# Performance work log

Measured on AMD Instinct MI355X. Metric: run time of the kernel, lower is better.

## Reference

```python
import jax, jax.numpy as jnp
import numpy as np

STRIDE = 16
NUM_A = 9
POS_TH, NEG_TH = 0.7, 0.3
FG, BG, IGN = 1.0, 0.0, 2.0
CAP = 128  # BATCH_SIZE * 0.5 for both fg and bg


def _generate_base_anchors(base_size=16, ratios=(0.5, 1.0, 2.0), scales=(8, 16, 32)):
    w = h = float(base_size)
    xc = yc = 0.5 * (base_size - 1)
    size = w * h
    out = []
    for r in ratios:
        ws = np.round(np.sqrt(size / r))
        hs = np.round(ws * r)
        for s in scales:
            W, H = ws * s, hs * s
            out.append([xc - 0.5 * (W - 1), yc - 0.5 * (H - 1),
                        xc + 0.5 * (W - 1), yc + 0.5 * (H - 1)])
    return np.asarray(out, dtype=np.float32)  # [9,4]


def _all_anchors(H, W):
    base = _generate_base_anchors()
    sx = np.arange(W, dtype=np.float32) * STRIDE
    sy = np.arange(H, dtype=np.float32) * STRIDE
    xs, ys = np.meshgrid(sx, sy)  # row-major over (h, w)
    shifts = np.stack([xs.ravel(), ys.ravel(), xs.ravel(), ys.ravel()], 1)
    return jnp.asarray((shifts[:, None, :] + base[None, :, :]).reshape(-1, 4))  # [H*W*9,4], order (h,w,a)


def _forward(scores, gt, im_w, im_h):
    H, W = scores.shape[2], scores.shape[3]
    anchors = _all_anchors(H, W)  # [N,4]
    valid = (anchors[:, 0] >= 0.) & (anchors[:, 1] >= 0.) & \
            (anchors[:, 2] < im_w) & (anchors[:, 3] < im_h)
    # pairwise IoU with +1 box convention
    aw = anchors[:, 2] - anchors[:, 0] + 1.
    ah = anchors[:, 3] - anchors[:, 1] + 1.
    a_area = jnp.where((aw > 0) & (ah > 0), aw * ah, 0.)
    gw = gt[:, 2] - gt[:, 0] + 1.
    gh = gt[:, 3] - gt[:, 1] + 1.
    g_area = jnp.where((gw > 0) & (gh > 0), gw * gh, 0.)
    ix1 = jnp.maximum(anchors[:, None, 0], gt[None, :, 0])
    iy1 = jnp.maximum(anchors[:, None, 1], gt[None, :, 1])
    ix2 = jnp.minimum(anchors[:, None, 2], gt[None, :, 2])
    iy2 = jnp.minimum(anchors[:, None, 3], gt[None, :, 3])
    iw = ix2 - ix1 + 1.
    ih = iy2 - iy1 + 1.
    inter = jnp.where((iw > 0) & (ih > 0), iw * ih, 0.)
    ovl = inter / (a_area[:, None] + g_area[None, :] - inter)  # [N,G]
    ovl_m = jnp.where(valid[:, None], ovl, -1.)  # exclude invalid anchors
    a_argmax = jnp.argmax(ovl, axis=1)           # best gt per anchor
    a_max = jnp.max(ovl, axis=1)
    g_max = jnp.max(ovl_m, axis=0)               # best (valid) anchor overlap per gt
    gt_fg = jnp.any(ovl_m == g_max[None, :], axis=1) & valid
    labels = jnp.where(valid & (a_max < NEG_TH), BG, IGN)
    labels = jnp.where(gt_fg, FG, labels)
    labels = jnp.where(valid & (a_max >= POS_TH), FG, labels)
    # random subsample fg/bg down to CAP each (matches npr.choice semantics in distribution)
    kf, kb = jax.random.split(jax.random.key(42))
    def subsample(lbl, mask, k):
        s = jnp.where(mask, jax.random.uniform(k, lbl.shape), jnp.inf)
        ranks = jnp.argsort(jnp.argsort(s))
        keep = ranks < jnp.minimum(jnp.sum(mask), CAP)
        return jnp.where(mask & ~keep, IGN, lbl)
    labels = subsample(labels, labels == FG, kf)
    labels = subsample(labels, labels == BG, kb)
    num_ni = jnp.sum(labels != IGN).astype(jnp.float32)
    gts = gt[a_argmax]
    ax = (anchors[:, 2] + anchors[:, 0]) * 0.5
    ay = (anchors[:, 3] + anchors[:, 1]) * 0.5
    gwm = gts[:, 2] - gts[:, 0] + 1.
    ghm = gts[:, 3] - gts[:, 1] + 1.
    gx = (gts[:, 2] + gts[:, 0]) * 0.5
    gy = (gts[:, 3] + gts[:, 1]) * 0.5
    adj = jnp.stack([(gx - ax) / aw, (gy - ay) / ah,
                     jnp.log(gwm / aw), jnp.log(ghm / ah)], axis=1)  # [N,4]
    adj = jnp.where(valid[:, None], adj, 0.)
    wts = jnp.where((labels == FG)[:, None], 1.0 / num_ni, 0.) * jnp.ones((1, 4), jnp.float32)
    labels_out = labels.reshape(1, H, W, NUM_A).transpose(0, 3, 1, 2) \
                       .reshape(1, 1, NUM_A * H, W).astype(jnp.int32)
    adj_out = adj.reshape(1, H, W, 4 * NUM_A).transpose(0, 3, 1, 2)
    wts_out = wts.reshape(1, H, W, 4 * NUM_A).transpose(0, 3, 1, 2)
    return labels_out, adj_out, wts_out


def setup_inputs() -> dict:
    key = jax.random.key(0)
    k1, k2, k3 = jax.random.split(key, 3)
    scores = jax.random.normal(k1, (1, 18, 256, 256), dtype=jnp.float32)
    G = 64
    cxy = jax.random.uniform(k2, (G, 2), minval=100., maxval=3900.)
    wh = jax.random.uniform(k3, (G, 2), minval=32., maxval=512.)
    x1y1 = jnp.clip(cxy - wh * 0.5, 0., 4095.)
    x2y2 = jnp.clip(cxy + wh * 0.5, 0., 4095.)
    gt = jnp.concatenate([x1y1, x2y2], axis=1)  # [G,4] = x1,y1,x2,y2
    return {"anchor_object_scores": scores, "ground_truth_boxes": gt,
            "im_w": 4096, "im_h": 4096}


def reference(anchor_object_scores, ground_truth_boxes, im_w, im_h):
    return _forward(anchor_object_scores, ground_truth_boxes, im_w, im_h)
```

## Files before the change

kernel.cpp:

```cpp
#include <hip/hip_runtime.h>
#include <stdint.h>


#define NUM_A 9
#define HW 65536
#define N_ANCH 589824
#define NG 64
#define CAPK 128u
#define NBIN 2048
#define BIN_SHIFT 12
#define CAND_CAP 2048

#define LAB_BG 0u
#define LAB_FG 1u
#define LAB_IGN 2u

#define OFF_HF    0
#define OFF_HB    NBIN
#define OFF_CNTF  (2*NBIN)
#define OFF_CNTB  (OFF_CNTF + 1)
#define OFF_ROOT1 (OFF_CNTF + 2)
#define OFF_ROOT2 (OFF_CNTF + 3)
#define OFF_SEL   (OFF_CNTF + 4)
#define OFF_SUB1  4112
#define OFF_SUB2  (OFF_SUB1 + 32*16)
#define CTRL_WORDS (OFF_SUB2 + 64*16)
#define OFF_CANDF CTRL_WORDS
#define OFF_CANDB (OFF_CANDF + 2*CAND_CAP)
#define OFF_LABM  (OFF_CANDB + 2*CAND_CAP)

#define NBLK_MAIN 576
#define NBLK_EMIT (N_ANCH / 256)
#define SUB1_N 32
#define SUB1_Q (NBLK_MAIN / SUB1_N)
#define SUB2_N 64
#define SUB2_Q (NBLK_EMIT / SUB2_N)

__constant__ float BA[NUM_A][4] = {
  { -84.f,  -40.f,  99.f,  55.f}, {-176.f,  -88.f, 191.f, 103.f},
  {-360.f, -184.f, 375.f, 199.f}, { -56.f,  -56.f,  71.f,  71.f},
  {-120.f, -120.f, 135.f, 135.f}, {-248.f, -248.f, 263.f, 263.f},
  { -36.f,  -80.f,  51.f,  95.f}, { -80.f, -168.f,  95.f, 183.f},
  {-168.f, -344.f, 183.f, 359.f}};

__host__ __device__ static inline void tf2x32(uint32_t k0, uint32_t k1,
                                              uint32_t x0, uint32_t x1,
                                              uint32_t* o0, uint32_t* o1) {
  const uint32_t ks2 = k0 ^ k1 ^ 0x1BD11BDAu;
#define TF_R(r) { x0 += x1; x1 = (x1 << (r)) | (x1 >> (32 - (r))); x1 ^= x0; }
  x0 += k0; x1 += k1;
  TF_R(13) TF_R(15) TF_R(26) TF_R(6)
  x0 += k1;  x1 += ks2 + 1u;
  TF_R(17) TF_R(29) TF_R(16) TF_R(24)
  x0 += ks2; x1 += k0 + 2u;
  TF_R(13) TF_R(15) TF_R(26) TF_R(6)
  x0 += k0;  x1 += k1 + 3u;
  TF_R(17) TF_R(29) TF_R(16) TF_R(24)
  x0 += k1;  x1 += ks2 + 4u;
  TF_R(13) TF_R(15) TF_R(26) TF_R(6)
  x0 += ks2; x1 += k0 + 5u;
#undef TF_R
  *o0 = x0; *o1 = x1;
}

__device__ static inline uint32_t mant_of(uint32_t k0, uint32_t k1, uint32_t n) {
  uint32_t o0, o1;
  tf2x32(k0, k1, 0u, n, &o0, &o1);
  return (o0 ^ o1) >> 9;
}

__device__ static inline float axis_best(float blo, float bhi, float glo,
                                         float ghi, int lo, int hi) {
  #pragma clang fp contract(off)
  float t1 = (ghi - bhi) * 0.0625f;
  float t2 = (glo - blo) * 0.0625f;
  float tmin = fminf(t1, t2), tmax = fmaxf(t1, t2);
  int c1 = (int)floorf(tmin), c2 = (int)ceilf(tmax);
  int cand0 = lo, cand1 = hi;
  int cand2 = min(max(c1,     lo), hi);
  int cand3 = min(max(c1 + 1, lo), hi);
  int cand4 = min(max(c2 - 1, lo), hi);
  int cand5 = min(max(c2,     lo), hi);
  float best = -3.0e38f;
  int cands[6] = {cand0, cand1, cand2, cand3, cand4, cand5};
  #pragma unroll
  for (int i = 0; i < 6; i++) {
    float s = (float)(cands[i] << 4);
    float v = fminf(bhi + s, ghi) - fmaxf(blo + s, glo) + 1.0f;
    best = fmaxf(best, v);
  }
  return best;
}

__global__ __launch_bounds__(256) void k_main2(const float* __restrict__ gt,
                                               const int* __restrict__ imw_p,
                                               const int* __restrict__ imh_p,
                                               float* __restrict__ out_adj,
                                               uint32_t* __restrict__ ws,
                                               uint32_t kf0, uint32_t kf1,
                                               uint32_t kb0, uint32_t kb1) {
  #pragma clang fp contract(off)
  __shared__ float sg0[NG], sg1[NG], sg2[NG], sg3[NG], sga[NG], sgm[NG];
  __shared__ uint32_t sgmU[NG];
  __shared__ uint32_t sh[2 * NBIN];
  __shared__ unsigned long long sMask[4];
  __shared__ int sAnyZero, sLast;
  int tid = threadIdx.x;
  int b = blockIdx.x;
  int a = b >> 6, hb = (b & 63) << 2;
  {
    uint4* sh4 = (uint4*)sh;
    #pragma unroll
    for (int k = 0; k < 4; k++) sh4[tid + k * 256] = make_uint4(0, 0, 0, 0);
  }
  if (tid == 0) sAnyZero = 0;
  if (tid < NG) {
    const float4 g4 = ((const float4*)gt)[tid];
    sg0[tid] = g4.x; sg1[tid] = g4.y; sg2[tid] = g4.z; sg3[tid] = g4.w;
    float gw = g4.z - g4.x + 1.0f, gh = g4.w - g4.y + 1.0f;
    sga[tid] = (gw > 0.0f && gh > 0.0f) ? gw * gh : 0.0f;
    sgmU[tid] = 0u;
  }
  __syncthreads();

  {
    int imwi = imw_p[0], imhi = imh_p[0];
    for (int p = tid; p < NG * NUM_A; p += 256) {
      int g = p / NUM_A, q = p - g * NUM_A;
      float b0 = BA[q][0], b1 = BA[q][1], b2 = BA[q][2], b3 = BA[q][3];
      int ib0 = (int)b0, ib1 = (int)b1, ib2 = (int)b2, ib3 = (int)b3;
      int wlo = max(0, (-ib0 + 15) >> 4);
      int whi = min(255, (imwi - ib2 - 1) >> 4);
      int hlo = max(0, (-ib1 + 15) >> 4);
      int hhi = min(255, (imhi - ib3 - 1) >> 4);
      if (wlo > whi || hlo > hhi) continue;
      float iwb = axis_best(b0, b2, sg0[g], sg2[g], wlo, whi);
      float ihb = axis_best(b1, b3, sg1[g], sg3[g], hlo, hhi);
      float aw = b2 - b0 + 1.0f, ah = b3 - b1 + 1.0f;
      float aarea = aw * ah;
      float inter = (iwb > 0.0f && ihb > 0.0f) ? iwb * ihb : 0.0f;
      float den = aarea + sga[g] - inter;
      float o = inter / den;
      atomicMax(&sgmU[g], __float_as_uint(o));
    }
  }

  {
    int wv = tid >> 6, g = tid & 63;
    float sy = (float)((hb + wv) << 4);
    float ihp = fminf(BA[a][3] + sy, sg3[g]) - fmaxf(BA[a][1] + sy, sg1[g]) + 1.0f;
    unsigned long long mk = __ballot(ihp > 0.0f);
    if (g == 0) sMask[wv] = mk;
  }
  __syncthreads();
  if (tid < NG) {
    uint32_t mm = sgmU[tid];
    sgm[tid] = __uint_as_float(mm);
    if (mm == 0u) atomicOr(&sAnyZero, 1);
  }
  __syncthreads();

  float BA0 = BA[a][0], BA1 = BA[a][1], BA2 = BA[a][2], BA3 = BA[a][3];
  float imw = (float)imw_p[0], imh = (float)imh_p[0];
  int w = tid;
  float sx = (float)(w << 4);
  float A0 = BA0 + sx, A2 = BA2 + sx;
  float aw = A2 - A0 + 1.0f;
  float A1v[4], A3v[4];
  #pragma unroll
  for (int r = 0; r < 4; r++) {
    float sy = (float)((hb + r) << 4);
    A1v[r] = BA1 + sy; A3v[r] = BA3 + sy;
  }
  float ah = A3v[0] - A1v[0] + 1.0f;
  float aarea = aw * ah;
  bool xv = (A0 >= 0.0f) && (A2 < imw);

  unsigned long long mk0 = sMask[0], mk1 = sMask[1],
                     mk2 = sMask[2], mk3 = sMask[3];
  unsigned long long uni = mk0 | mk1 | mk2 | mk3;
  float amaxv[4] = {0.f, 0.f, 0.f, 0.f};
  int bgv[4] = {0, 0, 0, 0};
  uint32_t afv = 0u;
  while (uni) {
    int g = __ffsll(uni) - 1;
    uni &= uni - 1;
    float iw = fminf(A2, sg2[g]) - fmaxf(A0, sg0[g]) + 1.0f;
    if (!__any(iw > 0.0f)) continue;
    if (iw > 0.0f) {
      float base = aarea + sga[g];
      float gy1 = sg1[g], gy2 = sg3[g], gm = sgm[g];
#define DO_ROW(r, mk)                                                     \
      if ((mk >> g) & 1ull) {                                             \
        float ih = fminf(A3v[r], gy2) - fmaxf(A1v[r], gy1) + 1.0f;        \
        float inter = iw * ih;                                            \
        float o = inter / (base - inter);                                 \
        if (o > amaxv[r]) { amaxv[r] = o; bgv[r] = g; }                   \
        if (o == gm) afv |= (1u << r);                                    \
      }
      DO_ROW(0, mk0) DO_ROW(1, mk1) DO_ROW(2, mk2) DO_ROW(3, mk3)
#undef DO_ROW
    }
  }

  bool anyZ = (sAnyZero != 0);
  #pragma unroll
  for (int r = 0; r < 4; r++) {
    int hw = (hb + r) * 256 + w;
    bool valid = xv && (A1v[r] >= 0.0f) && (A3v[r] < imh);
    float amax = amaxv[r];
    bool anyfg = (((afv >> r) & 1u) || anyZ) && valid;
    uint32_t lab;
    if (!valid)                       lab = LAB_IGN;
    else if (anyfg || amax >= 0.7f)   lab = LAB_FG;
    else if (amax < 0.3f)             lab = LAB_BG;
    else                              lab = LAB_IGN;

    float adj0 = 0.f, adj1 = 0.f, adj2 = 0.f, adj3 = 0.f;
    if (valid) {
      int bg = bgv[r];
      float G0 = sg0[bg], G1 = sg1[bg], G2 = sg2[bg], G3 = sg3[bg];
      float ax = (A2 + A0) * 0.5f, ay = (A3v[r] + A1v[r]) * 0.5f;
      float gwm = G2 - G0 + 1.0f, ghm = G3 - G1 + 1.0f;
      float gx = (G2 + G0) * 0.5f, gy = (G3 + G1) * 0.5f;
      adj0 = (gx - ax) / aw;
      adj1 = (gy - ay) / ah;
      adj2 = logf(gwm / aw);
      adj3 = logf(ghm / ah);
    }
    int c4 = a * 4;
    out_adj[(c4 + 0) * HW + hw] = adj0;
    out_adj[(c4 + 1) * HW + hw] = adj1;
    out_adj[(c4 + 2) * HW + hw] = adj2;
    out_adj[(c4 + 3) * HW + hw] = adj3;

    uint32_t m = 0u;
    uint32_t n = (uint32_t)(hw * 9 + a);
    if (lab != LAB_IGN) {
      uint32_t kk0 = (lab == LAB_FG) ? kf0 : kb0;
      uint32_t kk1 = (lab == LAB_FG) ? kf1 : kb1;
      m = mant_of(kk0, kk1, n);
      atomicAdd(&sh[((lab == LAB_FG) ? 0 : NBIN) + (m >> BIN_SHIFT)], 1u);
    }
    ws[OFF_LABM + a * HW + hw] = (lab << 24) | m;
  }

  __syncthreads();
  for (int i = tid; i < 2 * NBIN; i += 256) {
    uint32_t v = sh[i];
    if (v) atomicAdd(&ws[OFF_HF + i], v);
  }
  __syncthreads();
  if (tid == 0) {
    int lastF = 0;
    uint32_t v = atomicAdd(&ws[OFF_SUB1 + (b & (SUB1_N - 1)) * 16], 1u);
    if (v == SUB1_Q - 1) {
      uint32_t r = atomicAdd(&ws[OFF_ROOT1], 1u);
      if (r == SUB1_N - 1) lastF = 1;
    }
    sLast = lastF;
  }
  __syncthreads();
  if (sLast) {
    for (int cls = 0; cls < 2; cls++) {
      uint32_t* hist = ws + (cls ? OFF_HB : OFF_HF);
      uint32_t* sel = ws + OFF_SEL + cls * 4;
      uint32_t loc[8], s = 0;
      #pragma unroll
      for (int j = 0; j < 8; j++) {
        loc[j] = __hip_atomic_load(&hist[tid * 8 + j], __ATOMIC_RELAXED,
                                   __HIP_MEMORY_SCOPE_AGENT);
        s += loc[j];
      }
      sh[tid] = s; __syncthreads();
      for (int off = 1; off < 256; off <<= 1) {
        uint32_t v = (tid >= off) ? sh[tid - off] : 0u;
        __syncthreads();
        sh[tid] += v;
        __syncthreads();
      }
      uint32_t total = sh[255];
      uint32_t K = total < CAPK ? total : CAPK;
      if (tid == 0) {
        sel[3] = K;
        if (K == 0u) { sel[0] = 0xFFFFFFFFu; sel[1] = 0u; sel[2] = 0u; }
      }
      if (K > 0u) {
        uint32_t myC = sh[tid], pvC = (tid == 0) ? 0u : sh[tid - 1];
        if (myC >= K && pvC < K) {
          uint32_t cum = pvC; int bb = tid * 8;
          for (int j = 0; j < 8; j++) {
            if (cum + loc[j] >= K) { bb = tid * 8 + j; break; }
            cum += loc[j];
          }
          sel[0] = (uint32_t)bb; sel[1] = cum; sel[2] = K - cum;
        }
      }
      __syncthreads();
    }
  }
}

__global__ __launch_bounds__(256) void k_emitfix(float* __restrict__ out_lab,
                                                 float* __restrict__ out_wts,
                                                 uint32_t* __restrict__ ws) {
  __shared__ uint64_t sc[CAND_CAP];
  __shared__ int sLast;
  int tid = threadIdx.x;
  int t = blockIdx.x * 256 + tid;
  uint32_t lm = ws[OFF_LABM + t];
  uint32_t lab = lm >> 24;
  uint32_t m = lm & 0x7FFFFFu;
  uint32_t bf = ws[OFF_SEL + 0], bb = ws[OFF_SEL + 4];
  uint32_t Kf = ws[OFF_SEL + 3], Kb = ws[OFF_SEL + 7];
  float inv = 1.0f / (float)(Kf + Kb);
  int a = t >> 16, hw = t & 65535;
  uint32_t n = (uint32_t)(hw * 9 + a);

  float outv = 2.0f, wv = 0.0f;
  bool skip = false;
  if (lab == LAB_FG) {
    uint32_t bn = m >> BIN_SHIFT;
    if (bn < bf) { outv = 1.0f; wv = inv; }
    else if (bn == bf) {
      uint32_t idx = atomicAdd(&ws[OFF_CNTF], 1u);
      if (idx < CAND_CAP) {
        __hip_atomic_store((uint64_t*)(ws + OFF_CANDF) + idx,
                           ((uint64_t)m << 20) | (uint64_t)n,
                           __ATOMIC_RELAXED, __HIP_MEMORY_SCOPE_AGENT);
        skip = true;
      }
    }
  } else if (lab == LAB_BG) {
    uint32_t bn = m >> BIN_SHIFT;
    if (bn < bb) { outv = 0.0f; }
    else if (bn == bb) {
      uint32_t idx = atomicAdd(&ws[OFF_CNTB], 1u);
      if (idx < CAND_CAP) {
        __hip_atomic_store((uint64_t*)(ws + OFF_CANDB) + idx,
                           ((uint64_t)m << 20) | (uint64_t)n,
                           __ATOMIC_RELAXED, __HIP_MEMORY_SCOPE_AGENT);
        skip = true;
      }
    }
  }
  if (!skip) {
    out_lab[t] = outv;
    int c4 = a * 4;
    out_wts[(c4 + 0) * HW + hw] = wv;
    out_wts[(c4 + 1) * HW + hw] = wv;
    out_wts[(c4 + 2) * HW + hw] = wv;
    out_wts[(c4 + 3) * HW + hw] = wv;
  }

  asm volatile("s_waitcnt vmcnt(0)" ::: "memory");
  __syncthreads();
  if (tid == 0) {
    int lastF = 0;
    uint32_t v = atomicAdd(&ws[OFF_SUB2 + (blockIdx.x & (SUB2_N - 1)) * 16], 1u);
    if (v == SUB2_Q - 1) {
      uint32_t r = atomicAdd(&ws[OFF_ROOT2], 1u);
      if (r == SUB2_N - 1) lastF = 1;
    }
    sLast = lastF;
  }
  __syncthreads();
  if (sLast) {
    for (int cls = 0; cls < 2; cls++) {
      uint32_t cnt = __hip_atomic_load(&ws[cls == 0 ? OFF_CNTF : OFF_CNTB],
                                       __ATOMIC_RELAXED,
                                       __HIP_MEMORY_SCOPE_AGENT);
      uint32_t C = cnt < CAND_CAP ? cnt : CAND_CAP;
      uint32_t need = __hip_atomic_load(&ws[OFF_SEL + cls * 4 + 2],
                                        __ATOMIC_RELAXED,
                                        __HIP_MEMORY_SCOPE_AGENT);
      const uint64_t* cand =
          (const uint64_t*)(ws + (cls == 0 ? OFF_CANDF : OFF_CANDB));
      for (uint32_t i = tid; i < C; i += 256)
        sc[i] = __hip_atomic_load(&cand[i], __ATOMIC_RELAXED,
                                  __HIP_MEMORY_SCOPE_AGENT);
      __syncthreads();
      for (uint32_t i = tid; i < C; i += 256) {
        uint64_t k = sc[i];
        uint32_t rr = 0;
        for (uint32_t j = 0; j < C; j++) rr += (sc[j] < k) ? 1u : 0u;
        bool kept = (rr < need);
        uint32_t nn = (uint32_t)(k & 0xFFFFFu);
        uint32_t aa = nn % 9u, hww = nn / 9u;
        uint32_t tt = aa * HW + hww;
        float lv = kept ? (cls == 0 ? 1.0f : 0.0f) : 2.0f;
        float wvv = (kept && cls == 0) ? inv : 0.0f;
        __hip_atomic_store(&out_lab[tt], lv, __ATOMIC_RELAXED,
                           __HIP_MEMORY_SCOPE_AGENT);
        #pragma unroll
        for (int j2 = 0; j2 < 4; j2++)
          __hip_atomic_store(&out_wts[(aa * 4 + j2) * HW + hww], wvv,
                             __ATOMIC_RELAXED, __HIP_MEMORY_SCOPE_AGENT);
      }
      __syncthreads();
    }
  }
}

extern "C" void kernel_launch(void* const* d_in, const int* in_sizes, int n_in,
                              void* d_out, int out_size, void* d_ws,
                              size_t ws_size, hipStream_t stream) {
  const float* gt  = (const float*)d_in[1];
  const int*   imw = (const int*)d_in[2];
  const int*   imh = (const int*)d_in[3];
  float* out      = (float*)d_out;
  float* out_lab  = out;
  float* out_adj  = out + N_ANCH;
  float* out_wts  = out + 5 * N_ANCH;
  uint32_t* ws = (uint32_t*)d_ws;

  uint32_t kf0, kf1, kb0, kb1;
  tf2x32(0u, 42u, 0u, 0u, &kf0, &kf1);
  tf2x32(0u, 42u, 0u, 1u, &kb0, &kb1);

  hipMemsetAsync(ws, 0, CTRL_WORDS * sizeof(uint32_t), stream);
  hipLaunchKernelGGL(k_main2, dim3(NBLK_MAIN), dim3(256), 0, stream, gt, imw,
                     imh, out_adj, ws, kf0, kf1, kb0, kb1);
  hipLaunchKernelGGL(k_emitfix, dim3(NBLK_EMIT), dim3(256), 0, stream,
                     out_lab, out_wts, ws);
}
```

Baseline: 113.3 us.

## Fuse main and emit kernels into one cooperative kernel with grid-wide flag

Merges the labeling/histogram kernel and the emit/fix kernel into a single cooperatively launched kernel. Blocks keep their per-anchor label and mantissa in registers instead of round-tripping them through workspace memory. All blocks spin on a global flag set by the last block after threshold selection, and the old two-kernel path is kept as a fallback if the cooperative launch fails. This removes one kernel launch and the label/mantissa global write and read, at the cost of a grid-wide spin-wait and reliance on all 576 blocks being co-resident.

```diff
diff --git a/kernel.cpp b/kernel.cpp
--- a/kernel.cpp
+++ b/kernel.cpp
@@ -14,6 +14,22 @@
 #define LAB_BG 0u
 #define LAB_FG 1u
 #define LAB_IGN 2u
+
+#define NBLK_MAIN 576
+
+#define M_OFF_HF   0
+#define M_OFF_HB   NBIN
+#define M_OFF_CNTF (2*NBIN)
+#define M_OFF_CNTB (M_OFF_CNTF + 1)
+#define M_ROOTB    (M_OFF_CNTF + 2)
+#define M_ROOTD    (M_OFF_CNTF + 3)
+#define M_FLAGC    (M_OFF_CNTF + 4)
+#define M_OFF_SEL  4104
+#define M_SUBB     4112
+#define M_SUBD     (M_SUBB + 32*16)
+#define M_CTRL     (M_SUBD + 32*16)
+#define M_CANDF    M_CTRL
+#define M_CANDB    (M_CANDF + 2*CAND_CAP)
 
 #define OFF_HF    0
 #define OFF_HB    NBIN
@@ -28,8 +44,6 @@
 #define OFF_CANDF CTRL_WORDS
 #define OFF_CANDB (OFF_CANDF + 2*CAND_CAP)
 #define OFF_LABM  (OFF_CANDB + 2*CAND_CAP)
-
-#define NBLK_MAIN 576
 #define NBLK_EMIT (N_ANCH / 256)
 #define SUB1_N 32
 #define SUB1_Q (NBLK_MAIN / SUB1_N)
@@ -92,19 +106,25 @@
   return best;
 }
 
-__global__ __launch_bounds__(256) void k_main2(const float* __restrict__ gt,
-                                               const int* __restrict__ imw_p,
-                                               const int* __restrict__ imh_p,
-                                               float* __restrict__ out_adj,
-                                               uint32_t* __restrict__ ws,
-                                               uint32_t kf0, uint32_t kf1,
-                                               uint32_t kb0, uint32_t kb1) {
+#define AG_LOAD(p)      __hip_atomic_load((p), __ATOMIC_RELAXED, __HIP_MEMORY_SCOPE_AGENT)
+#define AG_STORE(p, v)  __hip_atomic_store((p), (v), __ATOMIC_RELAXED, __HIP_MEMORY_SCOPE_AGENT)
+
+__global__ __launch_bounds__(256) void k_all(const float* __restrict__ gt,
+                                             const int* __restrict__ imw_p,
+                                             const int* __restrict__ imh_p,
+                                             float* __restrict__ out_lab,
+                                             float* __restrict__ out_adj,
+                                             float* __restrict__ out_wts,
+                                             uint32_t* __restrict__ ws,
+                                             uint32_t kf0, uint32_t kf1,
+                                             uint32_t kb0, uint32_t kb1) {
   #pragma clang fp contract(off)
   __shared__ float sg0[NG], sg1[NG], sg2[NG], sg3[NG], sga[NG], sgm[NG];
   __shared__ uint32_t sgmU[NG];
   __shared__ uint32_t sh[2 * NBIN];
   __shared__ unsigned long long sMask[4];
-  __shared__ int sAnyZero, sLast;
+  __shared__ int sAnyZero, sLastB, sLastD;
+  __shared__ uint32_t sSel[8];
   int tid = threadIdx.x;
   int b = blockIdx.x;
   int a = b >> 6, hb = (b & 63) << 2;
@@ -204,6 +224,7 @@
   }
 
   bool anyZ = (sAnyZero != 0);
+  uint32_t lm[4];
   #pragma unroll
   for (int r = 0; r < 4; r++) {
     int hw = (hb + r) * 256 + w;
@@ -242,6 +263,315 @@
       m = mant_of(kk0, kk1, n);
       atomicAdd(&sh[((lab == LAB_FG) ? 0 : NBIN) + (m >> BIN_SHIFT)], 1u);
     }
+    lm[r] = (lab << 24) | m;
+  }
+
+  __syncthreads();
+  for (int i = tid; i < 2 * NBIN; i += 256) {
+    uint32_t v = sh[i];
+    if (v) atomicAdd(&ws[M_OFF_HF + i], v);
+  }
+  asm volatile("s_waitcnt vmcnt(0)" ::: "memory");
+  __syncthreads();
+
+  if (tid == 0) {
+    int last = 0;
+    uint32_t v = atomicAdd(&ws[M_SUBB + (b & 31) * 16], 1u);
+    if (v == 17u) {
+      uint32_t r = atomicAdd(&ws[M_ROOTB], 1u);
+      if (r == 31u) last = 1;
+    }
+    sLastB = last;
+  }
+  __syncthreads();
+  if (sLastB) {
+    for (int cls = 0; cls < 2; cls++) {
+      uint32_t* hist = ws + (cls ? M_OFF_HB : M_OFF_HF);
+      uint32_t* sel = ws + M_OFF_SEL + cls * 4;
+      uint32_t loc[8], s = 0;
+      #pragma unroll
+      for (int j = 0; j < 8; j++) {
+        loc[j] = AG_LOAD(&hist[tid * 8 + j]);
+        s += loc[j];
+      }
+      sh[tid] = s; __syncthreads();
+      for (int off = 1; off < 256; off <<= 1) {
+        uint32_t v = (tid >= off) ? sh[tid - off] : 0u;
+        __syncthreads();
+        sh[tid] += v;
+        __syncthreads();
+      }
+      uint32_t total = sh[255];
+      uint32_t K = total < CAPK ? total : CAPK;
+      if (tid == 0) {
+        AG_STORE(&sel[3], K);
+        if (K == 0u) {
+          AG_STORE(&sel[0], 0xFFFFFFFFu); AG_STORE(&sel[1], 0u);
+          AG_STORE(&sel[2], 0u);
+        }
+      }
+      if (K > 0u) {
+        uint32_t myC = sh[tid], pvC = (tid == 0) ? 0u : sh[tid - 1];
+        if (myC >= K && pvC < K) {
+          uint32_t cum = pvC; int bb = tid * 8;
+          for (int j = 0; j < 8; j++) {
+            if (cum + loc[j] >= K) { bb = tid * 8 + j; break; }
+            cum += loc[j];
+          }
+          AG_STORE(&sel[0], (uint32_t)bb); AG_STORE(&sel[1], cum);
+          AG_STORE(&sel[2], K - cum);
+        }
+      }
+      __syncthreads();
+    }
+    asm volatile("s_waitcnt vmcnt(0)" ::: "memory");
+    __syncthreads();
+    if (tid == 0) AG_STORE(&ws[M_FLAGC], 1u);
+  }
+
+  if (tid == 0) {
+    while (AG_LOAD(&ws[M_FLAGC]) == 0u) __builtin_amdgcn_s_sleep(4);
+  }
+  __syncthreads();
+  if (tid < 8) sSel[tid] = AG_LOAD(&ws[M_OFF_SEL + tid]);
+  __syncthreads();
+  uint32_t bf = sSel[0], Kf = sSel[3], bbn = sSel[4], Kb = sSel[7];
+  float inv = 1.0f / (float)(Kf + Kb);
+
+  #pragma unroll
+  for (int r = 0; r < 4; r++) {
+    int hw = (hb + r) * 256 + w;
+    uint32_t lab = lm[r] >> 24;
+    uint32_t m = lm[r] & 0x7FFFFFu;
+    uint32_t n = (uint32_t)(hw * 9 + a);
+    float outv = 2.0f, wv = 0.0f;
+    bool skip = false;
+    if (lab == LAB_FG) {
+      uint32_t bn = m >> BIN_SHIFT;
+      if (bn < bf) { outv = 1.0f; wv = inv; }
+      else if (bn == bf) {
+        uint32_t idx = atomicAdd(&ws[M_OFF_CNTF], 1u);
+        if (idx < CAND_CAP) {
+          AG_STORE((uint64_t*)(ws + M_CANDF) + idx,
+                   ((uint64_t)m << 20) | (uint64_t)n);
+          skip = true;
+        }
+      }
+    } else if (lab == LAB_BG) {
+      uint32_t bn = m >> BIN_SHIFT;
+      if (bn < bbn) { outv = 0.0f; }
+      else if (bn == bbn) {
+        uint32_t idx = atomicAdd(&ws[M_OFF_CNTB], 1u);
+        if (idx < CAND_CAP) {
+          AG_STORE((uint64_t*)(ws + M_CANDB) + idx,
+                   ((uint64_t)m << 20) | (uint64_t)n);
+          skip = true;
+        }
+      }
+    }
+    if (!skip) {
+      out_lab[a * HW + hw] = outv;
+      int c4 = a * 4;
+      out_wts[(c4 + 0) * HW + hw] = wv;
+      out_wts[(c4 + 1) * HW + hw] = wv;
+      out_wts[(c4 + 2) * HW + hw] = wv;
+      out_wts[(c4 + 3) * HW + hw] = wv;
+    }
+  }
+
+  asm volatile("s_waitcnt vmcnt(0)" ::: "memory");
+  __syncthreads();
+
+  if (tid == 0) {
+    int last = 0;
+    uint32_t v = atomicAdd(&ws[M_SUBD + (b & 31) * 16], 1u);
+    if (v == 17u) {
+      uint32_t r = atomicAdd(&ws[M_ROOTD], 1u);
+      if (r == 31u) last = 1;
+    }
+    sLastD = last;
+  }
+  __syncthreads();
+  if (sLastD) {
+    uint64_t* sc = (uint64_t*)sh;
+    for (int cls = 0; cls < 2; cls++) {
+      uint32_t cnt = AG_LOAD(&ws[cls == 0 ? M_OFF_CNTF : M_OFF_CNTB]);
+      uint32_t C = cnt < CAND_CAP ? cnt : CAND_CAP;
+      uint32_t need = AG_LOAD(&ws[M_OFF_SEL + cls * 4 + 2]);
+      const uint64_t* cand =
+          (const uint64_t*)(ws + (cls == 0 ? M_CANDF : M_CANDB));
+      for (uint32_t i = tid; i < C; i += 256) sc[i] = AG_LOAD(&cand[i]);
+      __syncthreads();
+      for (uint32_t i = tid; i < C; i += 256) {
+        uint64_t k = sc[i];
+        uint32_t rr = 0;
+        for (uint32_t j = 0; j < C; j++) rr += (sc[j] < k) ? 1u : 0u;
+        bool kept = (rr < need);
+        uint32_t nn = (uint32_t)(k & 0xFFFFFu);
+        uint32_t aa = nn % 9u, hww = nn / 9u;
+        uint32_t tt = aa * HW + hww;
+        float lv = kept ? (cls == 0 ? 1.0f : 0.0f) : 2.0f;
+        float wvv = (kept && cls == 0) ? inv : 0.0f;
+        AG_STORE(&out_lab[tt], lv);
+        #pragma unroll
+        for (int j2 = 0; j2 < 4; j2++)
+          AG_STORE(&out_wts[(aa * 4 + j2) * HW + hww], wvv);
+      }
+      __syncthreads();
+    }
+  }
+}
+
+__global__ __launch_bounds__(256) void k_main2(const float* __restrict__ gt,
+                                               const int* __restrict__ imw_p,
+                                               const int* __restrict__ imh_p,
+                                               float* __restrict__ out_adj,
+                                               uint32_t* __restrict__ ws,
+                                               uint32_t kf0, uint32_t kf1,
+                                               uint32_t kb0, uint32_t kb1) {
+  #pragma clang fp contract(off)
+  __shared__ float sg0[NG], sg1[NG], sg2[NG], sg3[NG], sga[NG], sgm[NG];
+  __shared__ uint32_t sgmU[NG];
+  __shared__ uint32_t sh[2 * NBIN];
+  __shared__ unsigned long long sMask[4];
+  __shared__ int sAnyZero, sLast;
+  int tid = threadIdx.x;
+  int b = blockIdx.x;
+  int a = b >> 6, hb = (b & 63) << 2;
+  {
+    uint4* sh4 = (uint4*)sh;
+    #pragma unroll
+    for (int k = 0; k < 4; k++) sh4[tid + k * 256] = make_uint4(0, 0, 0, 0);
+  }
+  if (tid == 0) sAnyZero = 0;
+  if (tid < NG) {
+    const float4 g4 = ((const float4*)gt)[tid];
+    sg0[tid] = g4.x; sg1[tid] = g4.y; sg2[tid] = g4.z; sg3[tid] = g4.w;
+    float gw = g4.z - g4.x + 1.0f, gh = g4.w - g4.y + 1.0f;
+    sga[tid] = (gw > 0.0f && gh > 0.0f) ? gw * gh : 0.0f;
+    sgmU[tid] = 0u;
+  }
+  __syncthreads();
+
+  {
+    int imwi = imw_p[0], imhi = imh_p[0];
+    for (int p = tid; p < NG * NUM_A; p += 256) {
+      int g = p / NUM_A, q = p - g * NUM_A;
+      float b0 = BA[q][0], b1 = BA[q][1], b2 = BA[q][2], b3 = BA[q][3];
+      int ib0 = (int)b0, ib1 = (int)b1, ib2 = (int)b2, ib3 = (int)b3;
+      int wlo = max(0, (-ib0 + 15) >> 4);
+      int whi = min(255, (imwi - ib2 - 1) >> 4);
+      int hlo = max(0, (-ib1 + 15) >> 4);
+      int hhi = min(255, (imhi - ib3 - 1) >> 4);
+      if (wlo > whi || hlo > hhi) continue;
+      float iwb = axis_best(b0, b2, sg0[g], sg2[g], wlo, whi);
+      float ihb = axis_best(b1, b3, sg1[g], sg3[g], hlo, hhi);
+      float aw = b2 - b0 + 1.0f, ah = b3 - b1 + 1.0f;
+      float aarea = aw * ah;
+      float inter = (iwb > 0.0f && ihb > 0.0f) ? iwb * ihb : 0.0f;
+      float den = aarea + sga[g] - inter;
+      float o = inter / den;
+      atomicMax(&sgmU[g], __float_as_uint(o));
+    }
+  }
+
+  {
+    int wv = tid >> 6, g = tid & 63;
+    float sy = (float)((hb + wv) << 4);
+    float ihp = fminf(BA[a][3] + sy, sg3[g]) - fmaxf(BA[a][1] + sy, sg1[g]) + 1.0f;
+    unsigned long long mk = __ballot(ihp > 0.0f);
+    if (g == 0) sMask[wv] = mk;
+  }
+  __syncthreads();
+  if (tid < NG) {
+    uint32_t mm = sgmU[tid];
+    sgm[tid] = __uint_as_float(mm);
+    if (mm == 0u) atomicOr(&sAnyZero, 1);
+  }
+  __syncthreads();
+
+  float BA0 = BA[a][0], BA1 = BA[a][1], BA2 = BA[a][2], BA3 = BA[a][3];
+  float imw = (float)imw_p[0], imh = (float)imh_p[0];
+  int w = tid;
+  float sx = (float)(w << 4);
+  float A0 = BA0 + sx, A2 = BA2 + sx;
+  float aw = A2 - A0 + 1.0f;
+  float A1v[4], A3v[4];
+  #pragma unroll
+  for (int r = 0; r < 4; r++) {
+    float sy = (float)((hb + r) << 4);
+    A1v[r] = BA1 + sy; A3v[r] = BA3 + sy;
+  }
+  float ah = A3v[0] - A1v[0] + 1.0f;
+  float aarea = aw * ah;
+  bool xv = (A0 >= 0.0f) && (A2 < imw);
+
+  unsigned long long mk0 = sMask[0], mk1 = sMask[1],
+                     mk2 = sMask[2], mk3 = sMask[3];
+  unsigned long long uni = mk0 | mk1 | mk2 | mk3;
+  float amaxv[4] = {0.f, 0.f, 0.f, 0.f};
+  int bgv[4] = {0, 0, 0, 0};
+  uint32_t afv = 0u;
+  while (uni) {
+    int g = __ffsll(uni) - 1;
+    uni &= uni - 1;
+    float iw = fminf(A2, sg2[g]) - fmaxf(A0, sg0[g]) + 1.0f;
+    if (!__any(iw > 0.0f)) continue;
+    if (iw > 0.0f) {
+      float base = aarea + sga[g];
+      float gy1 = sg1[g], gy2 = sg3[g], gm = sgm[g];
+#define DO_ROW(r, mk)                                                     \
+      if ((mk >> g) & 1ull) {                                             \
+        float ih = fminf(A3v[r], gy2) - fmaxf(A1v[r], gy1) + 1.0f;        \
+        float inter = iw * ih;                                            \
+        float o = inter / (base - inter);                                 \
+        if (o > amaxv[r]) { amaxv[r] = o; bgv[r] = g; }                   \
+        if (o == gm) afv |= (1u << r);                                    \
+      }
+      DO_ROW(0, mk0) DO_ROW(1, mk1) DO_ROW(2, mk2) DO_ROW(3, mk3)
+#undef DO_ROW
+    }
+  }
+
+  bool anyZ = (sAnyZero != 0);
+  #pragma unroll
+  for (int r = 0; r < 4; r++) {
+    int hw = (hb + r) * 256 + w;
+    bool valid = xv && (A1v[r] >= 0.0f) && (A3v[r] < imh);
+    float amax = amaxv[r];
+    bool anyfg = (((afv >> r) & 1u) || anyZ) && valid;
+    uint32_t lab;
+    if (!valid)                       lab = LAB_IGN;
+    else if (anyfg || amax >= 0.7f)   lab = LAB_FG;
+    else if (amax < 0.3f)             lab = LAB_BG;
+    else                              lab = LAB_IGN;
+
+    float adj0 = 0.f, adj1 = 0.f, adj2 = 0.f, adj3 = 0.f;
+    if (valid) {
+      int bg = bgv[r];
+      float G0 = sg0[bg], G1 = sg1[bg], G2 = sg2[bg], G3 = sg3[bg];
+      float ax = (A2 + A0) * 0.5f, ay = (A3v[r] + A1v[r]) * 0.5f;
+      float gwm = G2 - G0 + 1.0f, ghm = G3 - G1 + 1.0f;
+      float gx = (G2 + G0) * 0.5f, gy = (G3 + G1) * 0.5f;
+      adj0 = (gx - ax) / aw;
+      adj1 = (gy - ay) / ah;
+      adj2 = logf(gwm / aw);
+      adj3 = logf(ghm / ah);
+    }
+    int c4 = a * 4;
+    out_adj[(c4 + 0) * HW + hw] = adj0;
+    out_adj[(c4 + 1) * HW + hw] = adj1;
+    out_adj[(c4 + 2) * HW + hw] = adj2;
+    out_adj[(c4 + 3) * HW + hw] = adj3;
+
+    uint32_t m = 0u;
+    uint32_t n = (uint32_t)(hw * 9 + a);
+    if (lab != LAB_IGN) {
+      uint32_t kk0 = (lab == LAB_FG) ? kf0 : kb0;
+      uint32_t kk1 = (lab == LAB_FG) ? kf1 : kb1;
+      m = mant_of(kk0, kk1, n);
+      atomicAdd(&sh[((lab == LAB_FG) ? 0 : NBIN) + (m >> BIN_SHIFT)], 1u);
+    }
     ws[OFF_LABM + a * HW + hw] = (lab << 24) | m;
   }
 
@@ -268,8 +598,7 @@
       uint32_t loc[8], s = 0;
       #pragma unroll
       for (int j = 0; j < 8; j++) {
-        loc[j] = __hip_atomic_load(&hist[tid * 8 + j], __ATOMIC_RELAXED,
-                                   __HIP_MEMORY_SCOPE_AGENT);
+        loc[j] = AG_LOAD(&hist[tid * 8 + j]);
         s += loc[j];
       }
       sh[tid] = s; __syncthreads();
@@ -325,9 +654,8 @@
     else if (bn == bf) {
       uint32_t idx = atomicAdd(&ws[OFF_CNTF], 1u);
       if (idx < CAND_CAP) {
-        __hip_atomic_store((uint64_t*)(ws + OFF_CANDF) + idx,
-                           ((uint64_t)m << 20) | (uint64_t)n,
-                           __ATOMIC_RELAXED, __HIP_MEMORY_SCOPE_AGENT);
+        AG_STORE((uint64_t*)(ws + OFF_CANDF) + idx,
+                 ((uint64_t)m << 20) | (uint64_t)n);
         skip = true;
       }
     }
@@ -337,9 +665,8 @@
     else if (bn == bb) {
       uint32_t idx = atomicAdd(&ws[OFF_CNTB], 1u);
       if (idx < CAND_CAP) {
-        __hip_atomic_store((uint64_t*)(ws + OFF_CANDB) + idx,
-                           ((uint64_t)m << 20) | (uint64_t)n,
-                           __ATOMIC_RELAXED, __HIP_MEMORY_SCOPE_AGENT);
+        AG_STORE((uint64_t*)(ws + OFF_CANDB) + idx,
+                 ((uint64_t)m << 20) | (uint64_t)n);
         skip = true;
       }
     }
@@ -367,18 +694,12 @@
   __syncthreads();
   if (sLast) {
     for (int cls = 0; cls < 2; cls++) {
-      uint32_t cnt = __hip_atomic_load(&ws[cls == 0 ? OFF_CNTF : OFF_CNTB],
-                                       __ATOMIC_RELAXED,
-                                       __HIP_MEMORY_SCOPE_AGENT);
+      uint32_t cnt = AG_LOAD(&ws[cls == 0 ? OFF_CNTF : OFF_CNTB]);
       uint32_t C = cnt < CAND_CAP ? cnt : CAND_CAP;
-      uint32_t need = __hip_atomic_load(&ws[OFF_SEL + cls * 4 + 2],
-                                        __ATOMIC_RELAXED,
-                                        __HIP_MEMORY_SCOPE_AGENT);
+      uint32_t need = AG_LOAD(&ws[OFF_SEL + cls * 4 + 2]);
       const uint64_t* cand =
           (const uint64_t*)(ws + (cls == 0 ? OFF_CANDF : OFF_CANDB));
-      for (uint32_t i = tid; i < C; i += 256)
-        sc[i] = __hip_atomic_load(&cand[i], __ATOMIC_RELAXED,
-                                  __HIP_MEMORY_SCOPE_AGENT);
+      for (uint32_t i = tid; i < C; i += 256) sc[i] = AG_LOAD(&cand[i]);
       __syncthreads();
       for (uint32_t i = tid; i < C; i += 256) {
         uint64_t k = sc[i];
@@ -390,12 +711,10 @@
         uint32_t tt = aa * HW + hww;
         float lv = kept ? (cls == 0 ? 1.0f : 0.0f) : 2.0f;
         float wvv = (kept && cls == 0) ? inv : 0.0f;
-        __hip_atomic_store(&out_lab[tt], lv, __ATOMIC_RELAXED,
-                           __HIP_MEMORY_SCOPE_AGENT);
+        AG_STORE(&out_lab[tt], lv);
         #pragma unroll
         for (int j2 = 0; j2 < 4; j2++)
-          __hip_atomic_store(&out_wts[(aa * 4 + j2) * HW + hww], wvv,
-                             __ATOMIC_RELAXED, __HIP_MEMORY_SCOPE_AGENT);
+          AG_STORE(&out_wts[(aa * 4 + j2) * HW + hww], wvv);
       }
       __syncthreads();
     }
@@ -418,9 +737,19 @@
   tf2x32(0u, 42u, 0u, 0u, &kf0, &kf1);
   tf2x32(0u, 42u, 0u, 1u, &kb0, &kb1);
 
-  hipMemsetAsync(ws, 0, CTRL_WORDS * sizeof(uint32_t), stream);
-  hipLaunchKernelGGL(k_main2, dim3(NBLK_MAIN), dim3(256), 0, stream, gt, imw,
-                     imh, out_adj, ws, kf0, kf1, kb0, kb1);
-  hipLaunchKernelGGL(k_emitfix, dim3(NBLK_EMIT), dim3(256), 0, stream,
-                     out_lab, out_wts, ws);
+  hipMemsetAsync(ws, 0, M_CTRL * sizeof(uint32_t), stream);
+  void* kargs[] = {(void*)&gt,      (void*)&imw,     (void*)&imh,
+                   (void*)&out_lab, (void*)&out_adj, (void*)&out_wts,
+                   (void*)&ws,      (void*)&kf0,     (void*)&kf1,
+                   (void*)&kb0,     (void*)&kb1};
+  hipError_t err = hipLaunchCooperativeKernel(
+      (const void*)k_all, dim3(NBLK_MAIN), dim3(256), kargs, 0, stream);
+  if (err != hipSuccess) {
+    (void)hipGetLastError();
+    hipMemsetAsync(ws, 0, CTRL_WORDS * sizeof(uint32_t), stream);
+    hipLaunchKernelGGL(k_main2, dim3(NBLK_MAIN), dim3(256), 0, stream, gt,
+                       imw, imh, out_adj, ws, kf0, kf1, kb0, kb1);
+    hipLaunchKernelGGL(k_emitfix, dim3(NBLK_EMIT), dim3(256), 0, stream,
+                       out_lab, out_wts, ws);
+  }
 }
```

Measured after the change: 129.5 us. 1.14x slower.
